# Kernel optimization log

Measured on AMD Instinct MI355X. Metric: run time of the kernel, lower is better.

The kernel has to match this reference:

```python
import jax, jax.numpy as jnp
import numpy as np

IN_F = 256
OUT_F = 256
HOP = 3
ALPHA = 0.2   # LeakyReLU negative slope
BETA = 0.5    # hop mixing coefficient
N = 50000
E = 1600000


def setup_inputs() -> dict:
    key = jax.random.key(0)
    k1, k2, k3, k4 = jax.random.split(key, 4)
    inp = jax.random.normal(k1, (N, IN_F), dtype=jnp.float32)
    k_edge_list = jax.random.randint(k2, (HOP, 2, E), 0, N, dtype=jnp.int32)
    # xavier_normal-ish scales
    W = jax.random.normal(k3, (IN_F * HOP, OUT_F), dtype=jnp.float32) * (1.414 * np.sqrt(2.0 / (IN_F * HOP + OUT_F)))
    a = jax.random.normal(k4, (1, 2 * OUT_F * HOP), dtype=jnp.float32) * (1.414 * np.sqrt(2.0 / (1 + 2 * OUT_F * HOP)))
    return {"input": inp, "k_edge_list": k_edge_list, "W": W, "a": a}


def reference(input, k_edge_list, W, a):
    n = input.shape[0]
    h_prime_return = jnp.zeros((n, OUT_F), dtype=input.dtype)
    for i in range(HOP - 1, -1, -1):
        # per-hop projection: h = input @ W[i*in : (i+1)*in]  -> [N, OUT_F]
        h = input @ W[i * IN_F:(i + 1) * IN_F, :]
        src = k_edge_list[i, 0]  # [E] row indices (scatter targets)
        dst = k_edge_list[i, 1]  # [E] col indices (gather sources)
        ai = a[0, 2 * i * OUT_F:(2 * i + 2) * OUT_F]
        # a_i . cat(h[src], h[dst]) == (h @ a_src)[src] + (h @ a_dst)[dst]
        s_src = h @ ai[:OUT_F]   # [N]
        s_dst = h @ ai[OUT_F:]   # [N]
        score = s_src[src] + s_dst[dst]                     # [E]
        edge_e = jnp.exp(-jax.nn.leaky_relu(score, ALPHA))  # [E]
        # sparse row-sum: spmm(A, ones)
        e_rowsum = jax.ops.segment_sum(edge_e, src, num_segments=n)          # [N]
        # weighted aggregate: spmm(A, h)
        h_prime = jax.ops.segment_sum(edge_e[:, None] * h[dst], src, num_segments=n)  # [N, OUT_F]
        h_prime = h_prime / e_rowsum[:, None]
        h_prime_return = (1.0 - BETA) * h_prime + BETA * h_prime_return
    return jax.nn.elu(h_prime_return)  # concat=True path
```

## Files before the change

kernel.cpp:

```cpp
#include <hip/hip_runtime.h>

#define N_NODES 50000
#define E_EDGES 1600000
#define HOPS    3
#define KDIM    256
#define NOUT    768
#define MPAD    50048
#define NPS     50176
#define NCB     196
#define NCB_ALL (NCB * HOPS)
#define HSTRIDE ((size_t)MPAD * 256)
#define FCAP    12288
#define SEB     4096

typedef unsigned short u16;
typedef __bf16 bf16x8 __attribute__((ext_vector_type(8)));
typedef float  f32x4  __attribute__((ext_vector_type(4)));

__device__ __forceinline__ u16 f2bf(float f) {
  unsigned u = __float_as_uint(f);
  u += 0x7fffu + ((u >> 16) & 1u);
  return (u16)(u >> 16);
}
__device__ __forceinline__ float bf2f(u16 h) {
  return __uint_as_float(((unsigned)h) << 16);
}

__device__ __forceinline__ void gl2lds16(const void* g, void* l) {
  __builtin_amdgcn_global_load_lds(
      (__attribute__((address_space(1))) void*)(g),
      (__attribute__((address_space(3))) void*)(l), 16, 0, 0);
}

__global__ __launch_bounds__(256) void conv_a(const float* __restrict__ in,
                                              u16* __restrict__ A) {
  int idx  = blockIdx.x * 256 + threadIdx.x;
  int base = idx * 4;
  int row  = base >> 8;
  ushort4 o;
  if (row < N_NODES) {
    float4 v = *(const float4*)(in + base);
    o.x = f2bf(v.x); o.y = f2bf(v.y); o.z = f2bf(v.z); o.w = f2bf(v.w);
  } else {
    o.x = 0; o.y = 0; o.z = 0; o.w = 0;
  }
  *(ushort4*)(A + base) = o;
}

__global__ __launch_bounds__(256) void conv_w(const float* __restrict__ W,
                                              u16* __restrict__ Bt) {
  __shared__ float tile[32][33];
  int h  = blockIdx.z;
  int c0 = blockIdx.x * 32;
  int k0 = blockIdx.y * 32;
  int x  = threadIdx.x & 31;
  int y0 = threadIdx.x >> 5;
#pragma unroll
  for (int i = 0; i < 4; ++i) {
    int k = k0 + y0 + i * 8;
    tile[y0 + i * 8][x] = W[(size_t)(h * 256 + k) * 256 + (c0 + x)];
  }
  __syncthreads();
#pragma unroll
  for (int i = 0; i < 4; ++i) {
    int c = c0 + y0 + i * 8;
    Bt[(size_t)(h * 256 + c) * 256 + (k0 + x)] = f2bf(tile[x][y0 + i * 8]);
  }
}

__global__ __launch_bounds__(256) void gemm_kernel(const u16* __restrict__ A,
                                                   const u16* __restrict__ B,
                                                   u16* __restrict__ H,
                                                   const float* __restrict__ a,
                                                   float* __restrict__ ssrc,
                                                   float* __restrict__ sdst) {
  __shared__ char lds[16384];
  char* As = lds;
  char* Bs = lds + 8192;
  int tid  = threadIdx.x;
  int lane = tid & 63;
  int w    = tid >> 6;
  int wm   = w >> 1, wn = w & 1;
  int r    = lane & 15, q = lane >> 4;
  int bm   = blockIdx.y * 128, bn = blockIdx.x * 128;

  const u16* Ag0 = A + (size_t)(bm + 2 * w * 16 + r) * KDIM + q * 8;
  const u16* Bg0 = B + (size_t)(bn + 2 * w * 16 + r) * KDIM + q * 8;

  f32x4 zero = {0.f, 0.f, 0.f, 0.f};
  f32x4 acc[4][4];
#pragma unroll
  for (int mt = 0; mt < 4; ++mt)
#pragma unroll
    for (int nt = 0; nt < 4; ++nt) acc[mt][nt] = zero;

  for (int kt = 0; kt < 8; ++kt) {
    int ko = kt * 32;
    gl2lds16(Ag0 + ko,            As + (2 * w) * 1024);
    gl2lds16(Ag0 + 16 * KDIM + ko, As + (2 * w + 1) * 1024);
    gl2lds16(Bg0 + ko,            Bs + (2 * w) * 1024);
    gl2lds16(Bg0 + 16 * KDIM + ko, Bs + (2 * w + 1) * 1024);
    __syncthreads();
    bf16x8 af[4], bfv[4];
#pragma unroll
    for (int mt = 0; mt < 4; ++mt)
      af[mt] = *(const bf16x8*)(As + (wm * 4 + mt) * 1024 + lane * 16);
#pragma unroll
    for (int nt = 0; nt < 4; ++nt)
      bfv[nt] = *(const bf16x8*)(Bs + (wn * 4 + nt) * 1024 + lane * 16);
#pragma unroll
    for (int mt = 0; mt < 4; ++mt)
#pragma unroll
      for (int nt = 0; nt < 4; ++nt)
        acc[mt][nt] = __builtin_amdgcn_mfma_f32_16x16x32_bf16(
            af[mt], bfv[nt], acc[mt][nt], 0, 0, 0);
    __syncthreads();
  }

  int hop = bn >> 8;
  int cbase = (bn & 255) + wn * 64 + r;
  float asv[4], adv[4];
#pragma unroll
  for (int nt = 0; nt < 4; ++nt) {
    asv[nt] = a[hop * 512 + cbase + nt * 16];
    adv[nt] = a[hop * 512 + 256 + cbase + nt * 16];
  }
#pragma unroll
  for (int mt = 0; mt < 4; ++mt)
#pragma unroll
    for (int rg = 0; rg < 4; ++rg) {
      float ps = 0.f, pd = 0.f;
#pragma unroll
      for (int nt = 0; nt < 4; ++nt) {
        float v = acc[mt][nt][rg];
        ps += v * asv[nt];
        pd += v * adv[nt];
      }
#pragma unroll
      for (int m = 1; m < 16; m <<= 1) {
        ps += __shfl_xor(ps, m);
        pd += __shfl_xor(pd, m);
      }
      if (r == 0) {
        int row = bm + wm * 64 + mt * 16 + q * 4 + rg;
        if (row < N_NODES) {
          atomicAdd(&ssrc[hop * NPS + row], ps);
          atomicAdd(&sdst[hop * NPS + row], pd);
        }
      }
    }

#pragma unroll
  for (int mt = 0; mt < 4; ++mt)
#pragma unroll
    for (int nt = 0; nt < 4; ++nt)
#pragma unroll
      for (int rg = 0; rg < 4; ++rg) {
        int row = bm + wm * 64 + mt * 16 + q * 4 + rg;
        int col = bn + wn * 64 + nt * 16 + r;
        int c = col & 255;
        H[hop * HSTRIDE + (size_t)row * 256 + c] = f2bf(acc[mt][nt][rg]);
      }
}

__global__ __launch_bounds__(256) void count_kernel(const int* __restrict__ kel,
                                                    int* __restrict__ cc) {
  __shared__ int h[NCB];
  int t = threadIdx.x, hop = blockIdx.y;
  for (int i = t; i < NCB; i += 256) h[i] = 0;
  __syncthreads();
  const int* srcp = kel + (size_t)hop * 2 * E_EDGES;
  int e0 = blockIdx.x * SEB;
#pragma unroll
  for (int i = 0; i < 16; ++i) {
    int e = e0 + i * 256 + t;
    if (e < E_EDGES) atomicAdd(&h[srcp[e] >> 8], 1);
  }
  __syncthreads();
  for (int i = t; i < NCB; i += 256)
    if (h[i]) atomicAdd(&cc[hop * NCB + i], h[i]);
}

__global__ __launch_bounds__(256) void coarse_scan(const int* __restrict__ cc,
                                                   int* __restrict__ coff,
                                                   int* __restrict__ ccur) {
  __shared__ int wtot[4], wbase[4];
  int t = threadIdx.x, lane = t & 63, wv = t >> 6;
  int v[4];
  int s = 0;
#pragma unroll
  for (int i = 0; i < 4; ++i) {
    int idx = t * 4 + i;
    v[i] = (idx < NCB_ALL) ? cc[idx] : 0;
    s += v[i];
  }
  int ts = s;
#pragma unroll
  for (int d = 1; d < 64; d <<= 1) {
    int x = __shfl_up(s, d);
    if (lane >= d) s += x;
  }
  if (lane == 63) wtot[wv] = s;
  __syncthreads();
  if (t == 0) {
    int r = 0;
#pragma unroll
    for (int i = 0; i < 4; ++i) { wbase[i] = r; r += wtot[i]; }
  }
  __syncthreads();
  int ex = wbase[wv] + s - ts;
#pragma unroll
  for (int i = 0; i < 4; ++i) {
    int idx = t * 4 + i;
    if (idx < NCB_ALL) { coff[idx] = ex; ccur[idx] = ex; }
    ex += v[i];
  }
}

__global__ __launch_bounds__(256) void split1_kernel(const int* __restrict__ kel,
                                                     const float* __restrict__ ssrc,
                                                     const float* __restrict__ sdst,
                                                     int* __restrict__ ccur,
                                                     int2* __restrict__ packed) {
  __shared__ int2 stage[SEB];
  __shared__ int h[NCB];
  __shared__ int lofs[NCB];
  __shared__ int bbase[NCB];
  __shared__ int lcur[NCB];
  int t = threadIdx.x, hop = blockIdx.y;
  for (int i = t; i < NCB; i += 256) { h[i] = 0; lcur[i] = 0; }
  __syncthreads();
  const int* srcp = kel + (size_t)hop * 2 * E_EDGES;
  const int* dstp = srcp + E_EDGES;
  int e0 = blockIdx.x * SEB;
  int total = E_EDGES - e0; if (total > SEB) total = SEB;
  int esrc[16], edst[16];
#pragma unroll
  for (int i = 0; i < 16; ++i) {
    int e = e0 + i * 256 + t;
    if (e < E_EDGES) {
      esrc[i] = srcp[e];
      edst[i] = dstp[e];
      atomicAdd(&h[esrc[i] >> 8], 1);
    } else {
      esrc[i] = -1;
    }
  }
  __syncthreads();
  for (int i = t; i < NCB; i += 256)
    if (h[i]) bbase[i] = atomicAdd(&ccur[hop * NCB + i], h[i]);
  if (t < 64) {
    int run = 0;
#pragma unroll
    for (int c = 0; c < 4; ++c) {
      int idx = c * 64 + t;
      int v = (idx < NCB) ? h[idx] : 0;
      int s = v;
#pragma unroll
      for (int d = 1; d < 64; d <<= 1) {
        int x = __shfl_up(s, d);
        if (t >= d) s += x;
      }
      if (idx < NCB) lofs[idx] = run + s - v;
      run += __shfl(s, 63);
    }
  }
  __syncthreads();
#pragma unroll
  for (int i = 0; i < 16; ++i) {
    if (esrc[i] < 0) continue;
    int src = esrc[i], dst = edst[i];
    float s = ssrc[hop * NPS + src] + sdst[hop * NPS + dst];
    float lr = s > 0.0f ? s : 0.2f * s;
    float ee = __expf(-lr);
    int bin = src >> 8;
    int rank = atomicAdd(&lcur[bin], 1);
    stage[lofs[bin] + rank] =
        make_int2((bin << 24) | ((src & 255) << 16) | dst, __float_as_int(ee));
  }
  __syncthreads();
  for (int i = t; i < total; i += 256) {
    int2 r = stage[i];
    int bin = (unsigned)r.x >> 24;
    int pos = bbase[bin] + (i - lofs[bin]);
    packed[pos] = make_int2(r.x & 0x00FFFFFF, r.y);
  }
}

__global__ __launch_bounds__(1024, 1) void fine_kernel(const int* __restrict__ coff,
                                                       const int* __restrict__ cc,
                                                       int2* __restrict__ packed,
                                                       int* __restrict__ offs,
                                                       int* __restrict__ counts) {
  __shared__ int2 stage[FCAP];
  __shared__ int h2[256];
  __shared__ int lc[256];
  __shared__ int wtot[4], wbase[4];
  int t = threadIdx.x;
  int b = blockIdx.x;
  int hop = b / NCB, bl = b % NCB;
  int base = coff[b];
  int cnt = cc[b];
  if (cnt > FCAP) cnt = FCAP;
  if (t < 256) h2[t] = 0;
  __syncthreads();
  for (int i = t; i < cnt; i += 1024) {
    int2 r = packed[base + i];
    stage[i] = r;
    atomicAdd(&h2[(r.x >> 16) & 255], 1);
  }
  __syncthreads();
  int v = 0, s = 0;
  if (t < 256) {
    int lane = t & 63;
    v = h2[t];
    s = v;
#pragma unroll
    for (int d = 1; d < 64; d <<= 1) {
      int x = __shfl_up(s, d);
      if (lane >= d) s += x;
    }
    if (lane == 63) wtot[t >> 6] = s;
  }
  __syncthreads();
  if (t == 0) {
    int r = 0;
#pragma unroll
    for (int i = 0; i < 4; ++i) { wbase[i] = r; r += wtot[i]; }
  }
  __syncthreads();
  if (t < 256) {
    int ex = wbase[t >> 6] + s - v;
    int node = hop * NPS + bl * 256 + t;
    offs[node] = base + ex;
    counts[node] = v;
    lc[t] = ex;
  }
  __syncthreads();
  for (int i = t; i < cnt; i += 1024) {
    int2 r = stage[i];
    int low = (r.x >> 16) & 255;
    int rank = atomicAdd(&lc[low], 1);
    packed[base + rank] = make_int2(r.x & 0xFFFF, r.y);
  }
}

__device__ __forceinline__ void accum8(float* a, float& rs, float ee, uint4 h) {
  rs += ee;
  a[0] += ee * __uint_as_float(h.x << 16);
  a[1] += ee * __uint_as_float(h.x & 0xffff0000u);
  a[2] += ee * __uint_as_float(h.y << 16);
  a[3] += ee * __uint_as_float(h.y & 0xffff0000u);
  a[4] += ee * __uint_as_float(h.z << 16);
  a[5] += ee * __uint_as_float(h.z & 0xffff0000u);
  a[6] += ee * __uint_as_float(h.w << 16);
  a[7] += ee * __uint_as_float(h.w & 0xffff0000u);
}

__global__ __launch_bounds__(256) void agg_all(const int* __restrict__ offs,
                                               const int* __restrict__ counts,
                                               const int2* __restrict__ packed,
                                               const u16* __restrict__ Hbf,
                                               float* __restrict__ out) {
  int lane = threadIdx.x & 63, wid = threadIdx.x >> 6;
  int half = lane >> 5, sub = lane & 31;
  int n = blockIdx.x * 4 + wid;
  if (n >= N_NODES) return;

  float r[8];
#pragma unroll
  for (int c = 0; c < 8; ++c) r[c] = 0.f;

#pragma unroll
  for (int hop = 0; hop < HOPS; ++hop) {
    const float wgt = hop == 0 ? 0.5f : (hop == 1 ? 0.25f : 0.125f);
    int start = offs[hop * NPS + n];
    int cnt = counts[hop * NPS + n];
    const int2* pk = packed + start;
    const u16* Hh = Hbf + hop * HSTRIDE + sub * 8;
    float a0[8], a1[8];
    float rs0 = 0.f, rs1 = 0.f;
#pragma unroll
    for (int c = 0; c < 8; ++c) { a0[c] = 0.f; a1[c] = 0.f; }

    int np = cnt >> 1;
    int j = 0;
    for (; j + 8 <= np; j += 8) {
      int2 p[8];
#pragma unroll
      for (int i = 0; i < 8; ++i) p[i] = pk[2 * (j + i) + half];
      uint4 h[8];
#pragma unroll
      for (int i = 0; i < 8; ++i) h[i] = *(const uint4*)(Hh + (size_t)p[i].x * 256);
#pragma unroll
      for (int i = 0; i < 8; ++i)
        accum8((i & 1) ? a1 : a0, (i & 1) ? rs1 : rs0, __int_as_float(p[i].y), h[i]);
    }
    for (; j < np; ++j) {
      int2 p = pk[2 * j + half];
      uint4 hv = *(const uint4*)(Hh + (size_t)p.x * 256);
      accum8(a0, rs0, __int_as_float(p.y), hv);
    }
    if (cnt & 1) {
      int2 p = pk[cnt - 1];
      float ee = half ? 0.f : __int_as_float(p.y);
      uint4 hv = *(const uint4*)(Hh + (size_t)p.x * 256);
      accum8(a1, rs1, ee, hv);
    }

    float rs = rs0 + rs1;
    rs += __shfl_xor(rs, 32);
    float inv = wgt / rs;
#pragma unroll
    for (int c = 0; c < 8; ++c) {
      float t = a0[c] + a1[c];
      t += __shfl_xor(t, 32);
      r[c] += t * inv;
    }
  }

  float* op = out + (size_t)n * 256 + sub * 8 + half * 4;
  float4 o;
  float v0 = r[half * 4 + 0], v1 = r[half * 4 + 1];
  float v2 = r[half * 4 + 2], v3 = r[half * 4 + 3];
  o.x = v0 > 0.f ? v0 : expm1f(v0);
  o.y = v1 > 0.f ? v1 : expm1f(v1);
  o.z = v2 > 0.f ? v2 : expm1f(v2);
  o.w = v3 > 0.f ? v3 : expm1f(v3);
  *(float4*)op = o;
}

extern "C" void kernel_launch(void* const* d_in, const int* in_sizes, int n_in,
                              void* d_out, int out_size, void* d_ws, size_t ws_size,
                              hipStream_t stream) {
  const float* input = (const float*)d_in[0];
  const int*   kel   = (const int*)d_in[1];
  const float* W     = (const float*)d_in[2];
  const float* a     = (const float*)d_in[3];
  float* out = (float*)d_out;

  char* ws = (char*)d_ws;
  size_t o = 0;
  u16* Abf = (u16*)(ws + o);   o += (size_t)MPAD * KDIM * 2;
  u16* Bt  = (u16*)(ws + o);   o += (size_t)NOUT * KDIM * 2;
  u16* Hbf = (u16*)(ws + o);   o += (size_t)MPAD * NOUT * 2;
  float* ssrc = (float*)(ws + o); o += (size_t)3 * NPS * 4;
  float* sdst = (float*)(ws + o); o += (size_t)3 * NPS * 4;
  int* counts = (int*)(ws + o);   o += (size_t)3 * NPS * 4;
  int* offs   = (int*)(ws + o);   o += (size_t)3 * NPS * 4;
  int* cc     = (int*)(ws + o);   o += 4096;
  int* coff   = (int*)(ws + o);   o += 4096;
  int* ccur   = (int*)(ws + o);   o += 4096;
  int2* packed = (int2*)(ws + o); o += (size_t)3 * E_EDGES * 8;

  hipMemsetAsync(cc, 0, NCB_ALL * 4, stream);
  hipMemsetAsync(ssrc, 0, (size_t)2 * 3 * NPS * 4, stream);

  conv_a<<<MPAD * KDIM / 1024, 256, 0, stream>>>(input, Abf);
  conv_w<<<dim3(8, 8, 3), 256, 0, stream>>>(W, Bt);
  gemm_kernel<<<dim3(NOUT / 128, MPAD / 128), 256, 0, stream>>>(Abf, Bt, Hbf,
                                                                a, ssrc, sdst);

  int nsplit = (E_EDGES + SEB - 1) / SEB;
  count_kernel<<<dim3(nsplit, 3), 256, 0, stream>>>(kel, cc);
  coarse_scan<<<1, 256, 0, stream>>>(cc, coff, ccur);
  split1_kernel<<<dim3(nsplit, 3), 256, 0, stream>>>(kel, ssrc, sdst, ccur, packed);
  fine_kernel<<<NCB_ALL, 1024, 0, stream>>>(coff, cc, packed, offs, counts);

  agg_all<<<N_NODES / 4 + 1, 256, 0, stream>>>(offs, counts, packed, Hbf, out);
}
```

Before: 661.7 us.

## Double-buffer GEMM LDS staging and split aggregation into three launches

The GEMM main loop now uses two LDS buffers, so the global-to-LDS copy for the next K tile is issued before the MFMAs on the current tile, and one barrier per iteration is dropped. LDS use per block doubles to 32KB, which may lower occupancy. Separately, the aggregation kernel takes a node range and is launched three times over thirds of the nodes, which adds launch overhead without an obvious benefit on a single stream.

```diff
diff --git a/kernel.cpp b/kernel.cpp
--- a/kernel.cpp
+++ b/kernel.cpp
@@ -74,9 +74,7 @@
                                                    const float* __restrict__ a,
                                                    float* __restrict__ ssrc,
                                                    float* __restrict__ sdst) {
-  __shared__ char lds[16384];
-  char* As = lds;
-  char* Bs = lds + 8192;
+  __shared__ char lds[32768];
   int tid  = threadIdx.x;
   int lane = tid & 63;
   int w    = tid >> 6;
@@ -94,13 +92,25 @@
 #pragma unroll
     for (int nt = 0; nt < 4; ++nt) acc[mt][nt] = zero;
 
+#define STAGE(b, kt)                                                      \
+  do {                                                                    \
+    int ko = (kt) * 32;                                                   \
+    char* As_ = lds + (b) * 16384;                                        \
+    char* Bs_ = As_ + 8192;                                               \
+    gl2lds16(Ag0 + ko,             As_ + (2 * w) * 1024);                 \
+    gl2lds16(Ag0 + 16 * KDIM + ko, As_ + (2 * w + 1) * 1024);             \
+    gl2lds16(Bg0 + ko,             Bs_ + (2 * w) * 1024);                 \
+    gl2lds16(Bg0 + 16 * KDIM + ko, Bs_ + (2 * w + 1) * 1024);             \
+  } while (0)
+
+  STAGE(0, 0);
+  __syncthreads();
+
   for (int kt = 0; kt < 8; ++kt) {
-    int ko = kt * 32;
-    gl2lds16(Ag0 + ko,            As + (2 * w) * 1024);
-    gl2lds16(Ag0 + 16 * KDIM + ko, As + (2 * w + 1) * 1024);
-    gl2lds16(Bg0 + ko,            Bs + (2 * w) * 1024);
-    gl2lds16(Bg0 + 16 * KDIM + ko, Bs + (2 * w + 1) * 1024);
-    __syncthreads();
+    int cur = kt & 1;
+    if (kt < 7) STAGE(cur ^ 1, kt + 1);
+    char* As = lds + cur * 16384;
+    char* Bs = As + 8192;
     bf16x8 af[4], bfv[4];
 #pragma unroll
     for (int mt = 0; mt < 4; ++mt)
@@ -114,8 +124,9 @@
       for (int nt = 0; nt < 4; ++nt)
         acc[mt][nt] = __builtin_amdgcn_mfma_f32_16x16x32_bf16(
             af[mt], bfv[nt], acc[mt][nt], 0, 0, 0);
-    __syncthreads();
-  }
+    if (kt < 7) __syncthreads();
+  }
+#undef STAGE
 
   int hop = bn >> 8;
   int cbase = (bn & 255) + wn * 64 + r;
@@ -361,11 +372,12 @@
                                                const int* __restrict__ counts,
                                                const int2* __restrict__ packed,
                                                const u16* __restrict__ Hbf,
-                                               float* __restrict__ out) {
+                                               float* __restrict__ out,
+                                               int n0, int n1) {
   int lane = threadIdx.x & 63, wid = threadIdx.x >> 6;
   int half = lane >> 5, sub = lane & 31;
-  int n = blockIdx.x * 4 + wid;
-  if (n >= N_NODES) return;
+  int n = n0 + blockIdx.x * 4 + wid;
+  if (n >= n1) return;
 
   float r[8];
 #pragma unroll
@@ -467,5 +479,7 @@
   split1_kernel<<<dim3(nsplit, 3), 256, 0, stream>>>(kel, ssrc, sdst, ccur, packed);
   fine_kernel<<<NCB_ALL, 1024, 0, stream>>>(coff, cc, packed, offs, counts);
 
-  agg_all<<<N_NODES / 4 + 1, 256, 0, stream>>>(offs, counts, packed, Hbf, out);
-}
+  agg_all<<<4167, 256, 0, stream>>>(offs, counts, packed, Hbf, out, 0, 16668);
+  agg_all<<<4167, 256, 0, stream>>>(offs, counts, packed, Hbf, out, 16668, 33336);
+  agg_all<<<4166, 256, 0, stream>>>(offs, counts, packed, Hbf, out, 33336, 50000);
+}
```

After: 685.3 us. +3.6%, slower.
